# Performance work log

Measured on AMD Instinct MI355X. Metric: run time of the kernel, lower is better.

Reference implementation:

```python
import jax, jax.numpy as jnp
import numpy as np

OBS_DIM, GOAL_DIM, NUM_SKILLS, ACTION_DIM = 256, 64, 16, 32
HIDDEN = 128
BATCH = 65536


def setup_inputs() -> dict:
    key = jax.random.key(0)
    ks = jax.random.split(key, 10)
    s = lambda k, shape, fan_in: jax.random.normal(k, shape, jnp.float32) * (1.0 / np.sqrt(fan_in))
    return {
        "obs": jax.random.normal(ks[0], (BATCH, OBS_DIM), jnp.float32),
        "goals": jax.random.normal(ks[1], (BATCH, GOAL_DIM), jnp.float32),
        # gate (AlphaNet) params
        "Wa1": s(ks[2], (OBS_DIM + GOAL_DIM, HIDDEN), OBS_DIM + GOAL_DIM),
        "ba1": jnp.zeros((HIDDEN,), jnp.float32),
        "Wa2": s(ks[3], (HIDDEN, NUM_SKILLS), HIDDEN),
        "ba2": jnp.zeros((NUM_SKILLS,), jnp.float32),
        # stacked executor params: [S, in, out]
        "W1": s(ks[4], (NUM_SKILLS, OBS_DIM, HIDDEN), OBS_DIM),
        "b1": jnp.zeros((NUM_SKILLS, HIDDEN), jnp.float32),
        "W2": s(ks[5], (NUM_SKILLS, HIDDEN, ACTION_DIM), HIDDEN),
        "b2": jnp.zeros((NUM_SKILLS, ACTION_DIM), jnp.float32),
    }


def reference(obs, goals, Wa1, ba1, Wa2, ba2, W1, b1, W2, b2):
    # gate: softmax(Linear(ReLU(Linear(cat(obs, goals)))))
    concat_input = jnp.concatenate([obs, goals], axis=-1)  # [B, O+G]
    ha = jax.nn.relu(concat_input @ Wa1 + ba1)             # [B, H]
    alphas = jax.nn.softmax(ha @ Wa2 + ba2, axis=-1)       # [B, S]

    # all experts as one grouped GEMM over stacked weights
    h = jax.nn.relu(jnp.einsum("bo,soh->bsh", obs, W1) + b1[None])  # [B, S, H]
    skill_outputs = jnp.einsum("bsh,sha->bsa", h, W2) + b2[None]    # [B, S, A]

    # weighted sum over skills
    mixed_action = jnp.einsum("bsa,bs->ba", skill_outputs, alphas)  # [B, A]
    return mixed_action, alphas
```

## Files before the change

### kernel.cpp

```cpp
#include <hip/hip_runtime.h>


typedef __attribute__((ext_vector_type(8))) short    bf16x8;
typedef __attribute__((ext_vector_type(4))) float    f32x4;
typedef __attribute__((ext_vector_type(4))) _Float16 f16x4;

#define GATE_W1_OFF   0
#define GATE_W2_OFF   81920
#define GATE_BYTES    86016
#define S_W1_STRIDE   528
#define S_W2_OFF      67584
#define S_W2_STRIDE   264
#define S_IMG         76032
#define SKILL_OFF     86016
#define LDS_BYTES     162048

__device__ __forceinline__ unsigned short f2bf(float f) {
  unsigned u = __builtin_bit_cast(unsigned, f);
  return (unsigned short)((u + 0x7FFFu + ((u >> 16) & 1u)) >> 16);
}

__device__ __forceinline__ bf16x8 pack_bf8(f32x4 a, f32x4 b) {
  bf16x8 r;
  r[0] = (short)f2bf(a[0]); r[1] = (short)f2bf(a[1]);
  r[2] = (short)f2bf(a[2]); r[3] = (short)f2bf(a[3]);
  r[4] = (short)f2bf(b[0]); r[5] = (short)f2bf(b[1]);
  r[6] = (short)f2bf(b[2]); r[7] = (short)f2bf(b[3]);
  return r;
}

#define RELU_SCALE_PACK(dst, v, av, z)                                   \
  {                                                                      \
    auto lo_ = __builtin_amdgcn_cvt_pkrtz((v)[0], (v)[1]);               \
    auto hi_ = __builtin_amdgcn_cvt_pkrtz((v)[2], (v)[3]);               \
    lo_ = __builtin_elementwise_max(lo_, z) * (av);                      \
    hi_ = __builtin_elementwise_max(hi_, z) * (av);                      \
    dst[0] = (_Float16)lo_[0]; dst[1] = (_Float16)lo_[1];                \
    dst[2] = (_Float16)hi_[0]; dst[3] = (_Float16)hi_[1];                \
  }

__global__ void prep_weights(const float* __restrict__ Wa1, const float* __restrict__ Wa2,
                             const float* __restrict__ W1,  const float* __restrict__ W2,
                             unsigned char* __restrict__ ws) {
  int i = blockIdx.x * 256 + threadIdx.x;
  if (i < 524288) {
    int s = i >> 15, r = i & 32767, h = r >> 8, o = r & 255;
    float v = W1[(s * 256 + o) * 128 + h];
    *(unsigned short*)(ws + SKILL_OFF + s * S_IMG + h * S_W1_STRIDE + 2 * o) = f2bf(v);
  } else if (i < 589824) {
    int j = i - 524288, s = j >> 12, r = j & 4095, a = r >> 7, h = r & 127;
    float v = W2[(s * 128 + h) * 32 + a];
    *(_Float16*)(ws + SKILL_OFF + s * S_IMG + S_W2_OFF + a * S_W2_STRIDE + 2 * h) =
        (_Float16)v;
  } else if (i < 630784) {
    int j = i - 589824, h = j / 320, o = j - h * 320;
    float v = Wa1[o * 128 + h];
    *(unsigned short*)(ws + GATE_W1_OFF + h * 640 +
                       ((2 * o) ^ ((h & 7) << 4))) = f2bf(v);
  } else if (i < 632832) {
    int j = i - 630784, n = j >> 7, h = j & 127;
    float v = Wa2[h * 16 + n];
    *(_Float16*)(ws + GATE_W2_OFF + n * 256 +
                 ((2 * h) ^ ((n & 7) << 3))) = (_Float16)v;
  }
}

__device__ __forceinline__ void stage_lin(const unsigned char* gsrc, unsigned char* ldst,
                                          int tid, int bytes) {
  for (int off = tid * 16; off < bytes; off += 512 * 16) {
    __builtin_amdgcn_global_load_lds(
        (const __attribute__((address_space(1))) unsigned int*)(const void*)(gsrc + off),
        (__attribute__((address_space(3))) unsigned int*)(void*)(ldst + off), 16, 0, 0);
  }
}

__global__ __launch_bounds__(512, 2)
void mop_fused(const float* __restrict__ obs, const float* __restrict__ goals,
               const float* __restrict__ ba1, const float* __restrict__ ba2,
               const float* __restrict__ b1,  const float* __restrict__ b2,
               const unsigned char* __restrict__ ws, float* __restrict__ dout) {
  extern __shared__ unsigned char smem[];
  const int tid  = threadIdx.x;
  const int lane = tid & 63;
  const int wave = tid >> 6;
  const int l15  = lane & 15;
  const int g    = lane >> 4;
  const int swz4 = (lane & 7) << 4;
  const int swz3 = (lane & 7) << 3;
  const int rowbase = blockIdx.x * 256 + wave * 32;

  float* out_mixed = dout;
  float* out_alpha = dout + 65536 * 32;

  const int lw1 = l15 * S_W1_STRIDE + 16 * g;
  const int lw2 = S_W2_OFF + l15 * S_W2_STRIDE + 8 * g;

  stage_lin(ws, smem, tid, GATE_BYTES);

  bf16x8 obsf[2][8];
  bf16x8 goalf[2][2];
  #pragma unroll
  for (int nb = 0; nb < 2; ++nb) {
    const float* rp = obs + (size_t)(rowbase + nb * 16 + l15) * 256 + 8 * g;
    #pragma unroll
    for (int t = 0; t < 8; ++t) {
      f32x4 a = *(const f32x4*)(rp + 32 * t);
      f32x4 c = *(const f32x4*)(rp + 32 * t + 4);
      obsf[nb][t] = pack_bf8(a, c);
    }
    const float* gp = goals + (size_t)(rowbase + nb * 16 + l15) * 64 + 8 * g;
    #pragma unroll
    for (int t = 0; t < 2; ++t) {
      f32x4 a = *(const f32x4*)(gp + 32 * t);
      f32x4 c = *(const f32x4*)(gp + 32 * t + 4);
      goalf[nb][t] = pack_bf8(a, c);
    }
  }

  __syncthreads();

  stage_lin(ws + SKILL_OFF, smem + GATE_BYTES, tid, S_IMG);

  f32x4 gacc[2][8];
  #pragma unroll
  for (int ht = 0; ht < 8; ++ht) {
    f32x4 bias = *(const f32x4*)(ba1 + 16 * ht + 4 * g);
    gacc[0][ht] = bias; gacc[1][ht] = bias;
  }
  #pragma unroll
  for (int t = 0; t < 10; ++t) {
    bf16x8 bf0 = (t < 8) ? obsf[0][t] : goalf[0][t - 8];
    bf16x8 bf1 = (t < 8) ? obsf[1][t] : goalf[1][t - 8];
    #pragma unroll
    for (int ht = 0; ht < 8; ++ht) {
      int row = 16 * ht + l15;
      bf16x8 af = *(const bf16x8*)(smem + GATE_W1_OFF + row * 640 +
                                   ((64 * t + 16 * g) ^ swz4));
      gacc[0][ht] = __builtin_amdgcn_mfma_f32_16x16x32_bf16(af, bf0, gacc[0][ht], 0, 0, 0);
      gacc[1][ht] = __builtin_amdgcn_mfma_f32_16x16x32_bf16(af, bf1, gacc[1][ht], 0, 0, 0);
    }
  }

  const auto zh = __builtin_amdgcn_cvt_pkrtz(0.f, 0.f);
  f32x4 alph[2];
  #pragma unroll
  for (int nb = 0; nb < 2; ++nb) {
    f32x4 lacc = *(const f32x4*)(ba2 + 4 * g);
    #pragma unroll
    for (int ht = 0; ht < 8; ++ht) {
      f32x4 v = gacc[nb][ht];
      f16x4 hf;
      {
        auto lo_ = __builtin_amdgcn_cvt_pkrtz(v[0], v[1]);
        auto hi_ = __builtin_amdgcn_cvt_pkrtz(v[2], v[3]);
        lo_ = __builtin_elementwise_max(lo_, zh);
        hi_ = __builtin_elementwise_max(hi_, zh);
        hf[0] = (_Float16)lo_[0]; hf[1] = (_Float16)lo_[1];
        hf[2] = (_Float16)hi_[0]; hf[3] = (_Float16)hi_[1];
      }
      f16x4 wf = *(const f16x4*)(smem + GATE_W2_OFF + l15 * 256 +
                                 ((32 * ht + 8 * g) ^ swz3));
      lacc = __builtin_amdgcn_mfma_f32_16x16x16f16(wf, hf, lacc, 0, 0, 0);
    }
    float m = fmaxf(fmaxf(lacc[0], lacc[1]), fmaxf(lacc[2], lacc[3]));
    m = fmaxf(m, __shfl_xor(m, 16, 64));
    m = fmaxf(m, __shfl_xor(m, 32, 64));
    f32x4 e;
    e[0] = __expf(lacc[0] - m); e[1] = __expf(lacc[1] - m);
    e[2] = __expf(lacc[2] - m); e[3] = __expf(lacc[3] - m);
    float ssum = e[0] + e[1] + e[2] + e[3];
    ssum += __shfl_xor(ssum, 16, 64);
    ssum += __shfl_xor(ssum, 32, 64);
    float inv = 1.0f / ssum;
    alph[nb] = e * inv;
    *(f32x4*)(out_alpha + (size_t)(rowbase + nb * 16 + l15) * 16 + 4 * g) = alph[nb];
  }

  __syncthreads();

  f32x4 macc[2][2] = {};
  for (int s = 0; s < 16; ++s) {
    const unsigned char* buf = smem + ((s & 1) ? 0 : GATE_BYTES);
    if (s < 15) {
      unsigned char* nbuf = smem + (((s + 1) & 1) ? 0 : GATE_BYTES);
      stage_lin(ws + SKILL_OFF + (size_t)(s + 1) * S_IMG, nbuf, tid, S_IMG);
    }
    const int asrc = ((s >> 2) << 4) | l15;
    float p0 = (s & 1) ? alph[0][1] : alph[0][0];
    float p1 = (s & 1) ? alph[0][3] : alph[0][2];
    float as0 = __shfl((s & 2) ? p1 : p0, asrc, 64);
    float q0 = (s & 1) ? alph[1][1] : alph[1][0];
    float q1 = (s & 1) ? alph[1][3] : alph[1][2];
    float as1 = __shfl((s & 2) ? q1 : q0, asrc, 64);
    const auto a0h = __builtin_amdgcn_cvt_pkrtz(as0, as0);
    const auto a1h = __builtin_amdgcn_cvt_pkrtz(as1, as1);

    f32x4 b1v[8];
    #pragma unroll
    for (int ht = 0; ht < 8; ++ht)
      b1v[ht] = *(const f32x4*)(b1 + s * 128 + 16 * ht + 4 * g);
    f32x4 b2v[2];
    #pragma unroll
    for (int ta = 0; ta < 2; ++ta)
      b2v[ta] = *(const f32x4*)(b2 + s * 32 + 16 * ta + 4 * g);

    const unsigned char* w1p = buf + lw1;
    const unsigned char* w2p = buf + lw2;

    __builtin_amdgcn_s_setprio(1);
    #pragma unroll
    for (int ht = 0; ht < 8; ++ht) {
      f32x4 acc0 = b1v[ht], acc1 = b1v[ht];
      #pragma unroll
      for (int t = 0; t < 8; ++t) {
        bf16x8 af = *(const bf16x8*)(w1p + ht * 8448 + t * 64);
        acc0 = __builtin_amdgcn_mfma_f32_16x16x32_bf16(af, obsf[0][t], acc0, 0, 0, 0);
        acc1 = __builtin_amdgcn_mfma_f32_16x16x32_bf16(af, obsf[1][t], acc1, 0, 0, 0);
      }
      f16x4 hf0, hf1;
      RELU_SCALE_PACK(hf0, acc0, a0h, zh);
      RELU_SCALE_PACK(hf1, acc1, a1h, zh);
      #pragma unroll
      for (int ta = 0; ta < 2; ++ta) {
        f16x4 wf = *(const f16x4*)(w2p + ta * 4224 + ht * 32);
        macc[0][ta] = __builtin_amdgcn_mfma_f32_16x16x16f16(wf, hf0, macc[0][ta], 0, 0, 0);
        macc[1][ta] = __builtin_amdgcn_mfma_f32_16x16x16f16(wf, hf1, macc[1][ta], 0, 0, 0);
      }
    }
    __builtin_amdgcn_s_setprio(0);
    #pragma unroll
    for (int ta = 0; ta < 2; ++ta) {
      macc[0][ta] = macc[0][ta] + b2v[ta] * as0;
      macc[1][ta] = macc[1][ta] + b2v[ta] * as1;
    }
    __syncthreads();
  }

  #pragma unroll
  for (int nb = 0; nb < 2; ++nb) {
    #pragma unroll
    for (int ta = 0; ta < 2; ++ta) {
      *(f32x4*)(out_mixed + (size_t)(rowbase + nb * 16 + l15) * 32 + 16 * ta + 4 * g) =
          macc[nb][ta];
    }
  }
}

extern "C" void kernel_launch(void* const* d_in, const int* in_sizes, int n_in,
                              void* d_out, int out_size, void* d_ws, size_t ws_size,
                              hipStream_t stream) {
  const float* obs   = (const float*)d_in[0];
  const float* goals = (const float*)d_in[1];
  const float* Wa1   = (const float*)d_in[2];
  const float* ba1   = (const float*)d_in[3];
  const float* Wa2   = (const float*)d_in[4];
  const float* ba2   = (const float*)d_in[5];
  const float* W1    = (const float*)d_in[6];
  const float* b1    = (const float*)d_in[7];
  const float* W2    = (const float*)d_in[8];
  const float* b2    = (const float*)d_in[9];
  unsigned char* ws  = (unsigned char*)d_ws;
  float* out = (float*)d_out;

  prep_weights<<<2472, 256, 0, stream>>>(Wa1, Wa2, W1, W2, ws);
  mop_fused<<<256, 512, LDS_BYTES, stream>>>(obs, goals, ba1, ba2, b1, b2, ws, out);
}
```

Before: 99.33 us.

## Register-block four row tiles per wave and halve block to four waves

Each wave now processes 64 rows (four 16-row tiles) instead of 32, and the block is halved to 256 threads. Each LDS weight fragment therefore feeds four MFMAs instead of two, cutting LDS read traffic per unit of compute. The W2 row stride in the LDS image is padded from 264 to 272 bytes to change the bank mapping, and the s_setprio hints are removed. The cost is much higher register use and only four waves per CU, which leaves less latency hiding for the LDS staging and global loads.

After: 113.9 us. +14.7%, slower.

```diff
diff --git a/kernel.cpp b/kernel.cpp
--- a/kernel.cpp
+++ b/kernel.cpp
@@ -4,16 +4,17 @@
 typedef __attribute__((ext_vector_type(8))) short    bf16x8;
 typedef __attribute__((ext_vector_type(4))) float    f32x4;
 typedef __attribute__((ext_vector_type(4))) _Float16 f16x4;
+using half2v = decltype(__builtin_amdgcn_cvt_pkrtz(0.f, 0.f));
 
 #define GATE_W1_OFF   0
 #define GATE_W2_OFF   81920
 #define GATE_BYTES    86016
 #define S_W1_STRIDE   528
 #define S_W2_OFF      67584
-#define S_W2_STRIDE   264
-#define S_IMG         76032
+#define S_W2_STRIDE   272
+#define S_IMG         76288
 #define SKILL_OFF     86016
-#define LDS_BYTES     162048
+#define LDS_BYTES     162304
 
 __device__ __forceinline__ unsigned short f2bf(float f) {
   unsigned u = __builtin_bit_cast(unsigned, f);
@@ -31,8 +32,8 @@
 
 #define RELU_SCALE_PACK(dst, v, av, z)                                   \
   {                                                                      \
-    auto lo_ = __builtin_amdgcn_cvt_pkrtz((v)[0], (v)[1]);               \
-    auto hi_ = __builtin_amdgcn_cvt_pkrtz((v)[2], (v)[3]);               \
+    half2v lo_ = __builtin_amdgcn_cvt_pkrtz((v)[0], (v)[1]);             \
+    half2v hi_ = __builtin_amdgcn_cvt_pkrtz((v)[2], (v)[3]);             \
     lo_ = __builtin_elementwise_max(lo_, z) * (av);                      \
     hi_ = __builtin_elementwise_max(hi_, z) * (av);                      \
     dst[0] = (_Float16)lo_[0]; dst[1] = (_Float16)lo_[1];                \
@@ -67,14 +68,14 @@
 
 __device__ __forceinline__ void stage_lin(const unsigned char* gsrc, unsigned char* ldst,
                                           int tid, int bytes) {
-  for (int off = tid * 16; off < bytes; off += 512 * 16) {
+  for (int off = tid * 16; off < bytes; off += 256 * 16) {
     __builtin_amdgcn_global_load_lds(
         (const __attribute__((address_space(1))) unsigned int*)(const void*)(gsrc + off),
         (__attribute__((address_space(3))) unsigned int*)(void*)(ldst + off), 16, 0, 0);
   }
 }
 
-__global__ __launch_bounds__(512, 2)
+__global__ __launch_bounds__(256, 1)
 void mop_fused(const float* __restrict__ obs, const float* __restrict__ goals,
                const float* __restrict__ ba1, const float* __restrict__ ba2,
                const float* __restrict__ b1,  const float* __restrict__ b2,
@@ -87,7 +88,7 @@
   const int g    = lane >> 4;
   const int swz4 = (lane & 7) << 4;
   const int swz3 = (lane & 7) << 3;
-  const int rowbase = blockIdx.x * 256 + wave * 32;
+  const int rowbase = blockIdx.x * 256 + wave * 64;
 
   float* out_mixed = dout;
   float* out_alpha = dout + 65536 * 32;
@@ -97,10 +98,10 @@
 
   stage_lin(ws, smem, tid, GATE_BYTES);
 
-  bf16x8 obsf[2][8];
-  bf16x8 goalf[2][2];
-  #pragma unroll
-  for (int nb = 0; nb < 2; ++nb) {
+  bf16x8 obsf[4][8];
+  bf16x8 goalf[4][2];
+  #pragma unroll
+  for (int nb = 0; nb < 4; ++nb) {
     const float* rp = obs + (size_t)(rowbase + nb * 16 + l15) * 256 + 8 * g;
     #pragma unroll
     for (int t = 0; t < 8; ++t) {
@@ -121,38 +122,41 @@
 
   stage_lin(ws + SKILL_OFF, smem + GATE_BYTES, tid, S_IMG);
 
-  f32x4 gacc[2][8];
+  f32x4 gacc[4][8];
   #pragma unroll
   for (int ht = 0; ht < 8; ++ht) {
     f32x4 bias = *(const f32x4*)(ba1 + 16 * ht + 4 * g);
-    gacc[0][ht] = bias; gacc[1][ht] = bias;
+    #pragma unroll
+    for (int nb = 0; nb < 4; ++nb) gacc[nb][ht] = bias;
   }
   #pragma unroll
   for (int t = 0; t < 10; ++t) {
-    bf16x8 bf0 = (t < 8) ? obsf[0][t] : goalf[0][t - 8];
-    bf16x8 bf1 = (t < 8) ? obsf[1][t] : goalf[1][t - 8];
+    bf16x8 bf[4];
+    #pragma unroll
+    for (int nb = 0; nb < 4; ++nb) bf[nb] = (t < 8) ? obsf[nb][t] : goalf[nb][t - 8];
     #pragma unroll
     for (int ht = 0; ht < 8; ++ht) {
       int row = 16 * ht + l15;
       bf16x8 af = *(const bf16x8*)(smem + GATE_W1_OFF + row * 640 +
                                    ((64 * t + 16 * g) ^ swz4));
-      gacc[0][ht] = __builtin_amdgcn_mfma_f32_16x16x32_bf16(af, bf0, gacc[0][ht], 0, 0, 0);
-      gacc[1][ht] = __builtin_amdgcn_mfma_f32_16x16x32_bf16(af, bf1, gacc[1][ht], 0, 0, 0);
-    }
-  }
-
-  const auto zh = __builtin_amdgcn_cvt_pkrtz(0.f, 0.f);
-  f32x4 alph[2];
-  #pragma unroll
-  for (int nb = 0; nb < 2; ++nb) {
+      #pragma unroll
+      for (int nb = 0; nb < 4; ++nb)
+        gacc[nb][ht] = __builtin_amdgcn_mfma_f32_16x16x32_bf16(af, bf[nb], gacc[nb][ht], 0, 0, 0);
+    }
+  }
+
+  const half2v zh = __builtin_amdgcn_cvt_pkrtz(0.f, 0.f);
+  f32x4 alph[4];
+  #pragma unroll
+  for (int nb = 0; nb < 4; ++nb) {
     f32x4 lacc = *(const f32x4*)(ba2 + 4 * g);
     #pragma unroll
     for (int ht = 0; ht < 8; ++ht) {
       f32x4 v = gacc[nb][ht];
       f16x4 hf;
       {
-        auto lo_ = __builtin_amdgcn_cvt_pkrtz(v[0], v[1]);
-        auto hi_ = __builtin_amdgcn_cvt_pkrtz(v[2], v[3]);
+        half2v lo_ = __builtin_amdgcn_cvt_pkrtz(v[0], v[1]);
+        half2v hi_ = __builtin_amdgcn_cvt_pkrtz(v[2], v[3]);
         lo_ = __builtin_elementwise_max(lo_, zh);
         hi_ = __builtin_elementwise_max(hi_, zh);
         hf[0] = (_Float16)lo_[0]; hf[1] = (_Float16)lo_[1];
@@ -178,7 +182,7 @@
 
   __syncthreads();
 
-  f32x4 macc[2][2] = {};
+  f32x4 macc[4][2] = {};
   for (int s = 0; s < 16; ++s) {
     const unsigned char* buf = smem + ((s & 1) ? 0 : GATE_BYTES);
     if (s < 15) {
@@ -186,14 +190,15 @@
       stage_lin(ws + SKILL_OFF + (size_t)(s + 1) * S_IMG, nbuf, tid, S_IMG);
     }
     const int asrc = ((s >> 2) << 4) | l15;
-    float p0 = (s & 1) ? alph[0][1] : alph[0][0];
-    float p1 = (s & 1) ? alph[0][3] : alph[0][2];
-    float as0 = __shfl((s & 2) ? p1 : p0, asrc, 64);
-    float q0 = (s & 1) ? alph[1][1] : alph[1][0];
-    float q1 = (s & 1) ? alph[1][3] : alph[1][2];
-    float as1 = __shfl((s & 2) ? q1 : q0, asrc, 64);
-    const auto a0h = __builtin_amdgcn_cvt_pkrtz(as0, as0);
-    const auto a1h = __builtin_amdgcn_cvt_pkrtz(as1, as1);
+    float av[4];
+    half2v ah[4];
+    #pragma unroll
+    for (int nb = 0; nb < 4; ++nb) {
+      float c0 = (s & 1) ? alph[nb][1] : alph[nb][0];
+      float c1 = (s & 1) ? alph[nb][3] : alph[nb][2];
+      av[nb] = __shfl((s & 2) ? c1 : c0, asrc, 64);
+      ah[nb] = __builtin_amdgcn_cvt_pkrtz(av[nb], av[nb]);
+    }
 
     f32x4 b1v[8];
     #pragma unroll
@@ -207,37 +212,40 @@
     const unsigned char* w1p = buf + lw1;
     const unsigned char* w2p = buf + lw2;
 
-    __builtin_amdgcn_s_setprio(1);
     #pragma unroll
     for (int ht = 0; ht < 8; ++ht) {
-      f32x4 acc0 = b1v[ht], acc1 = b1v[ht];
+      f32x4 acc[4];
+      #pragma unroll
+      for (int nb = 0; nb < 4; ++nb) acc[nb] = b1v[ht];
       #pragma unroll
       for (int t = 0; t < 8; ++t) {
         bf16x8 af = *(const bf16x8*)(w1p + ht * 8448 + t * 64);
-        acc0 = __builtin_amdgcn_mfma_f32_16x16x32_bf16(af, obsf[0][t], acc0, 0, 0, 0);
-        acc1 = __builtin_amdgcn_mfma_f32_16x16x32_bf16(af, obsf[1][t], acc1, 0, 0, 0);
+        #pragma unroll
+        for (int nb = 0; nb < 4; ++nb)
+          acc[nb] = __builtin_amdgcn_mfma_f32_16x16x32_bf16(af, obsf[nb][t], acc[nb], 0, 0, 0);
       }
-      f16x4 hf0, hf1;
-      RELU_SCALE_PACK(hf0, acc0, a0h, zh);
-      RELU_SCALE_PACK(hf1, acc1, a1h, zh);
+      f16x4 hf[4];
+      #pragma unroll
+      for (int nb = 0; nb < 4; ++nb) RELU_SCALE_PACK(hf[nb], acc[nb], ah[nb], zh);
       #pragma unroll
       for (int ta = 0; ta < 2; ++ta) {
-        f16x4 wf = *(const f16x4*)(w2p + ta * 4224 + ht * 32);
-        macc[0][ta] = __builtin_amdgcn_mfma_f32_16x16x16f16(wf, hf0, macc[0][ta], 0, 0, 0);
-        macc[1][ta] = __builtin_amdgcn_mfma_f32_16x16x16f16(wf, hf1, macc[1][ta], 0, 0, 0);
+        f16x4 wf = *(const f16x4*)(w2p + ta * 4352 + ht * 32);
+        #pragma unroll
+        for (int nb = 0; nb < 4; ++nb)
+          macc[nb][ta] = __builtin_amdgcn_mfma_f32_16x16x16f16(wf, hf[nb], macc[nb][ta], 0, 0, 0);
       }
     }
-    __builtin_amdgcn_s_setprio(0);
-    #pragma unroll
-    for (int ta = 0; ta < 2; ++ta) {
-      macc[0][ta] = macc[0][ta] + b2v[ta] * as0;
-      macc[1][ta] = macc[1][ta] + b2v[ta] * as1;
+    #pragma unroll
+    for (int nb = 0; nb < 4; ++nb) {
+      #pragma unroll
+      for (int ta = 0; ta < 2; ++ta)
+        macc[nb][ta] = macc[nb][ta] + b2v[ta] * av[nb];
     }
     __syncthreads();
   }
 
   #pragma unroll
-  for (int nb = 0; nb < 2; ++nb) {
+  for (int nb = 0; nb < 4; ++nb) {
     #pragma unroll
     for (int ta = 0; ta < 2; ++ta) {
       *(f32x4*)(out_mixed + (size_t)(rowbase + nb * 16 + l15) * 32 + 16 * ta + 4 * g) =
@@ -263,5 +271,5 @@
   float* out = (float*)d_out;
 
   prep_weights<<<2472, 256, 0, stream>>>(Wa1, Wa2, W1, W2, ws);
-  mop_fused<<<256, 512, LDS_BYTES, stream>>>(obs, goals, ba1, ba2, b1, b2, ws, out);
-}
+  mop_fused<<<256, 256, LDS_BYTES, stream>>>(obs, goals, ba1, ba2, b1, b2, ws, out);
+}
```

## Stage biases into LDS with weight images and use hardware bf16 pack

Applied to the files above, without the earlier changes.

Packs the gate and per-skill bias vectors into the prepared workspace images so they arrive in LDS with the weights through the existing async staging. The kernel then reads biases from LDS instead of global memory inside the skill loop. It also replaces the software bf16 rounding with the v_cvt_pk_bf16_f32 instruction and pads the W2 row stride from 264 to 272 bytes. The trade-off is a slightly larger LDS footprint and staged image, which could affect occupancy headroom.

After: 95.86 us. 3.5% less time.

```diff
diff --git a/kernel.cpp b/kernel.cpp
--- a/kernel.cpp
+++ b/kernel.cpp
@@ -4,16 +4,20 @@
 typedef __attribute__((ext_vector_type(8))) short    bf16x8;
 typedef __attribute__((ext_vector_type(4))) float    f32x4;
 typedef __attribute__((ext_vector_type(4))) _Float16 f16x4;
+using half2v = decltype(__builtin_amdgcn_cvt_pkrtz(0.f, 0.f));
 
 #define GATE_W1_OFF   0
 #define GATE_W2_OFF   81920
-#define GATE_BYTES    86016
+#define GATE_BA1_OFF  86016
+#define GATE_BA2_OFF  86528
+#define GATE_BYTES    86592
 #define S_W1_STRIDE   528
 #define S_W2_OFF      67584
-#define S_W2_STRIDE   264
-#define S_IMG         76032
-#define SKILL_OFF     86016
-#define LDS_BYTES     162048
+#define S_W2_STRIDE   272
+#define S_B1_OFF      76288
+#define S_B2_OFF      76800
+#define S_IMG         76928
+#define LDS_BYTES     163520
 
 __device__ __forceinline__ unsigned short f2bf(float f) {
   unsigned u = __builtin_bit_cast(unsigned, f);
@@ -21,18 +25,18 @@
 }
 
 __device__ __forceinline__ bf16x8 pack_bf8(f32x4 a, f32x4 b) {
-  bf16x8 r;
-  r[0] = (short)f2bf(a[0]); r[1] = (short)f2bf(a[1]);
-  r[2] = (short)f2bf(a[2]); r[3] = (short)f2bf(a[3]);
-  r[4] = (short)f2bf(b[0]); r[5] = (short)f2bf(b[1]);
-  r[6] = (short)f2bf(b[2]); r[7] = (short)f2bf(b[3]);
-  return r;
+  int4 r;
+  asm("v_cvt_pk_bf16_f32 %0, %1, %2" : "=v"(r.x) : "v"(a[0]), "v"(a[1]));
+  asm("v_cvt_pk_bf16_f32 %0, %1, %2" : "=v"(r.y) : "v"(a[2]), "v"(a[3]));
+  asm("v_cvt_pk_bf16_f32 %0, %1, %2" : "=v"(r.z) : "v"(b[0]), "v"(b[1]));
+  asm("v_cvt_pk_bf16_f32 %0, %1, %2" : "=v"(r.w) : "v"(b[2]), "v"(b[3]));
+  return __builtin_bit_cast(bf16x8, r);
 }
 
 #define RELU_SCALE_PACK(dst, v, av, z)                                   \
   {                                                                      \
-    auto lo_ = __builtin_amdgcn_cvt_pkrtz((v)[0], (v)[1]);               \
-    auto hi_ = __builtin_amdgcn_cvt_pkrtz((v)[2], (v)[3]);               \
+    half2v lo_ = __builtin_amdgcn_cvt_pkrtz((v)[0], (v)[1]);             \
+    half2v hi_ = __builtin_amdgcn_cvt_pkrtz((v)[2], (v)[3]);             \
     lo_ = __builtin_elementwise_max(lo_, z) * (av);                      \
     hi_ = __builtin_elementwise_max(hi_, z) * (av);                      \
     dst[0] = (_Float16)lo_[0]; dst[1] = (_Float16)lo_[1];                \
@@ -40,17 +44,19 @@
   }
 
 __global__ void prep_weights(const float* __restrict__ Wa1, const float* __restrict__ Wa2,
+                             const float* __restrict__ ba1, const float* __restrict__ ba2,
                              const float* __restrict__ W1,  const float* __restrict__ W2,
+                             const float* __restrict__ b1,  const float* __restrict__ b2,
                              unsigned char* __restrict__ ws) {
   int i = blockIdx.x * 256 + threadIdx.x;
   if (i < 524288) {
     int s = i >> 15, r = i & 32767, h = r >> 8, o = r & 255;
     float v = W1[(s * 256 + o) * 128 + h];
-    *(unsigned short*)(ws + SKILL_OFF + s * S_IMG + h * S_W1_STRIDE + 2 * o) = f2bf(v);
+    *(unsigned short*)(ws + GATE_BYTES + s * S_IMG + h * S_W1_STRIDE + 2 * o) = f2bf(v);
   } else if (i < 589824) {
     int j = i - 524288, s = j >> 12, r = j & 4095, a = r >> 7, h = r & 127;
     float v = W2[(s * 128 + h) * 32 + a];
-    *(_Float16*)(ws + SKILL_OFF + s * S_IMG + S_W2_OFF + a * S_W2_STRIDE + 2 * h) =
+    *(_Float16*)(ws + GATE_BYTES + s * S_IMG + S_W2_OFF + a * S_W2_STRIDE + 2 * h) =
         (_Float16)v;
   } else if (i < 630784) {
     int j = i - 589824, h = j / 320, o = j - h * 320;
@@ -62,6 +68,18 @@
     float v = Wa2[h * 16 + n];
     *(_Float16*)(ws + GATE_W2_OFF + n * 256 +
                  ((2 * h) ^ ((n & 7) << 3))) = (_Float16)v;
+  } else if (i < 634880) {
+    int j = i - 632832, s = j >> 7, h = j & 127;
+    *(float*)(ws + GATE_BYTES + s * S_IMG + S_B1_OFF + 4 * h) = b1[s * 128 + h];
+  } else if (i < 635392) {
+    int j = i - 634880, s = j >> 5, a = j & 31;
+    *(float*)(ws + GATE_BYTES + s * S_IMG + S_B2_OFF + 4 * a) = b2[s * 32 + a];
+  } else if (i < 635520) {
+    int j = i - 635392;
+    *(float*)(ws + GATE_BA1_OFF + 4 * j) = ba1[j];
+  } else if (i < 635536) {
+    int j = i - 635520;
+    *(float*)(ws + GATE_BA2_OFF + 4 * j) = ba2[j];
   }
 }
 
@@ -76,8 +94,6 @@
 
 __global__ __launch_bounds__(512, 2)
 void mop_fused(const float* __restrict__ obs, const float* __restrict__ goals,
-               const float* __restrict__ ba1, const float* __restrict__ ba2,
-               const float* __restrict__ b1,  const float* __restrict__ b2,
                const unsigned char* __restrict__ ws, float* __restrict__ dout) {
   extern __shared__ unsigned char smem[];
   const int tid  = threadIdx.x;
@@ -94,6 +110,7 @@
 
   const int lw1 = l15 * S_W1_STRIDE + 16 * g;
   const int lw2 = S_W2_OFF + l15 * S_W2_STRIDE + 8 * g;
+  const int lb  = 16 * g;
 
   stage_lin(ws, smem, tid, GATE_BYTES);
 
@@ -119,12 +136,12 @@
 
   __syncthreads();
 
-  stage_lin(ws + SKILL_OFF, smem + GATE_BYTES, tid, S_IMG);
+  stage_lin(ws + GATE_BYTES, smem + GATE_BYTES, tid, S_IMG);
 
   f32x4 gacc[2][8];
   #pragma unroll
   for (int ht = 0; ht < 8; ++ht) {
-    f32x4 bias = *(const f32x4*)(ba1 + 16 * ht + 4 * g);
+    f32x4 bias = *(const f32x4*)(smem + GATE_BA1_OFF + 64 * ht + lb);
     gacc[0][ht] = bias; gacc[1][ht] = bias;
   }
   #pragma unroll
@@ -141,18 +158,18 @@
     }
   }
 
-  const auto zh = __builtin_amdgcn_cvt_pkrtz(0.f, 0.f);
+  const half2v zh = __builtin_amdgcn_cvt_pkrtz(0.f, 0.f);
   f32x4 alph[2];
   #pragma unroll
   for (int nb = 0; nb < 2; ++nb) {
-    f32x4 lacc = *(const f32x4*)(ba2 + 4 * g);
+    f32x4 lacc = *(const f32x4*)(smem + GATE_BA2_OFF + lb);
     #pragma unroll
     for (int ht = 0; ht < 8; ++ht) {
       f32x4 v = gacc[nb][ht];
       f16x4 hf;
       {
-        auto lo_ = __builtin_amdgcn_cvt_pkrtz(v[0], v[1]);
-        auto hi_ = __builtin_amdgcn_cvt_pkrtz(v[2], v[3]);
+        half2v lo_ = __builtin_amdgcn_cvt_pkrtz(v[0], v[1]);
+        half2v hi_ = __builtin_amdgcn_cvt_pkrtz(v[2], v[3]);
         lo_ = __builtin_elementwise_max(lo_, zh);
         hi_ = __builtin_elementwise_max(hi_, zh);
         hf[0] = (_Float16)lo_[0]; hf[1] = (_Float16)lo_[1];
@@ -183,8 +200,17 @@
     const unsigned char* buf = smem + ((s & 1) ? 0 : GATE_BYTES);
     if (s < 15) {
       unsigned char* nbuf = smem + (((s + 1) & 1) ? 0 : GATE_BYTES);
-      stage_lin(ws + SKILL_OFF + (size_t)(s + 1) * S_IMG, nbuf, tid, S_IMG);
-    }
+      stage_lin(ws + GATE_BYTES + (size_t)(s + 1) * S_IMG, nbuf, tid, S_IMG);
+    }
+    f32x4 b1v[8];
+    #pragma unroll
+    for (int ht = 0; ht < 8; ++ht)
+      b1v[ht] = *(const f32x4*)(buf + S_B1_OFF + 64 * ht + lb);
+    f32x4 b2v[2];
+    #pragma unroll
+    for (int ta = 0; ta < 2; ++ta)
+      b2v[ta] = *(const f32x4*)(buf + S_B2_OFF + 64 * ta + lb);
+
     const int asrc = ((s >> 2) << 4) | l15;
     float p0 = (s & 1) ? alph[0][1] : alph[0][0];
     float p1 = (s & 1) ? alph[0][3] : alph[0][2];
@@ -192,17 +218,8 @@
     float q0 = (s & 1) ? alph[1][1] : alph[1][0];
     float q1 = (s & 1) ? alph[1][3] : alph[1][2];
     float as1 = __shfl((s & 2) ? q1 : q0, asrc, 64);
-    const auto a0h = __builtin_amdgcn_cvt_pkrtz(as0, as0);
-    const auto a1h = __builtin_amdgcn_cvt_pkrtz(as1, as1);
-
-    f32x4 b1v[8];
-    #pragma unroll
-    for (int ht = 0; ht < 8; ++ht)
-      b1v[ht] = *(const f32x4*)(b1 + s * 128 + 16 * ht + 4 * g);
-    f32x4 b2v[2];
-    #pragma unroll
-    for (int ta = 0; ta < 2; ++ta)
-      b2v[ta] = *(const f32x4*)(b2 + s * 32 + 16 * ta + 4 * g);
+    const half2v a0h = __builtin_amdgcn_cvt_pkrtz(as0, as0);
+    const half2v a1h = __builtin_amdgcn_cvt_pkrtz(as1, as1);
 
     const unsigned char* w1p = buf + lw1;
     const unsigned char* w2p = buf + lw2;
@@ -222,7 +239,7 @@
       RELU_SCALE_PACK(hf1, acc1, a1h, zh);
       #pragma unroll
       for (int ta = 0; ta < 2; ++ta) {
-        f16x4 wf = *(const f16x4*)(w2p + ta * 4224 + ht * 32);
+        f16x4 wf = *(const f16x4*)(w2p + ta * 4352 + ht * 32);
         macc[0][ta] = __builtin_amdgcn_mfma_f32_16x16x16f16(wf, hf0, macc[0][ta], 0, 0, 0);
         macc[1][ta] = __builtin_amdgcn_mfma_f32_16x16x16f16(wf, hf1, macc[1][ta], 0, 0, 0);
       }
@@ -262,6 +279,6 @@
   unsigned char* ws  = (unsigned char*)d_ws;
   float* out = (float*)d_out;
 
-  prep_weights<<<2472, 256, 0, stream>>>(Wa1, Wa2, W1, W2, ws);
-  mop_fused<<<256, 512, LDS_BYTES, stream>>>(obs, goals, ba1, ba2, b1, b2, ws, out);
-}
+  prep_weights<<<2483, 256, 0, stream>>>(Wa1, Wa2, ba1, ba2, W1, W2, b1, b2, ws);
+  mop_fused<<<256, 512, LDS_BYTES, stream>>>(obs, goals, ws, out);
+}
```
